# Kernel optimization log

Hardware: AMD Instinct MI355X
Metric: run time of the kernel (lower is better)

## Reference

```python
import math
import jax, jax.numpy as jnp
import numpy as np

B, S, D = 2, 2048, 512
H = 8
DPH = D // H
NEG = -1e18


def lorentz_linear(x, W, b, log_scale):
    """LorentzLinear with head_num=H: linear map then per-head projection onto the
    Lorentz hyperboloid: time = sigmoid(y0)*exp(scale)+1.1, space rescaled so that
    -time^2 + |space|^2 = -1 per head chunk."""
    Bx, Sx, Dx = x.shape
    y = (x @ W.T + b).reshape(Bx, Sx, H, DPH)
    time = jax.nn.sigmoid(y[..., :1]) * jnp.exp(log_scale) + 1.1
    space = y[..., 1:]
    sq = jnp.clip(jnp.sum(space * space, axis=-1, keepdims=True), 1e-8, None)
    scale = (time * time - 1.0) / sq
    out = jnp.concatenate([time, space * jnp.sqrt(scale)], axis=-1)
    return out.reshape(Bx, Sx, Dx)


def setup_inputs() -> dict:
    key0 = jax.random.key(0)
    ks = jax.random.split(key0, 8)
    std = 1.0 / np.sqrt(D)
    causal = ~jnp.tril(jnp.ones((S, S), dtype=bool))  # True = masked out
    return {
        "key": jax.random.normal(ks[0], (B, S, D), jnp.float32),
        "value": jax.random.normal(ks[1], (B, S, D), jnp.float32),
        "query": jax.random.normal(ks[2], (B, S, D), jnp.float32),
        "mask": jnp.broadcast_to(causal[None], (B, S, S)),
        "Wq": jax.random.normal(ks[3], (D, D), jnp.float32) * std,
        "bq": jnp.zeros((D,), jnp.float32),
        "sq": jnp.asarray(math.log(10.0), jnp.float32),
        "Wk": jax.random.normal(ks[4], (D, D), jnp.float32) * std,
        "bk": jnp.zeros((D,), jnp.float32),
        "sk": jnp.asarray(math.log(10.0), jnp.float32),
        "Wv": jax.random.normal(ks[5], (D, D), jnp.float32) * std,
        "bv": jnp.zeros((D,), jnp.float32),
        "sv": jnp.asarray(math.log(10.0), jnp.float32),
        "att_scale": jnp.full((1,), math.sqrt(D), jnp.float32),
        "att_bias": jnp.zeros((), jnp.float32),
    }


def reference(key, value, query, mask, Wq, bq, sq, Wk, bk, sk, Wv, bv, sv,
              att_scale, att_bias):
    def shape(x):  # (B,S,D) -> (B,H,S,dph)
        return x.reshape(B, -1, H, DPH).transpose(0, 2, 1, 3)

    q = shape(lorentz_linear(query, Wq, bq, sq))
    k = shape(lorentz_linear(key, Wk, bk, sk))
    v = shape(lorentz_linear(value, Wv, bv, sv))

    # Lorentz inner product <q,k>_L = -q0*k0 + q_space . k_space
    qm = jnp.concatenate([-q[..., :1], q[..., 1:]], axis=-1)
    cin = jnp.einsum('bhqd,bhkd->bhqk', qm, k)
    scores = (2.0 + 2.0 * cin) / att_scale + att_bias
    scores = jnp.where(mask[:, None], NEG, scores)
    attn = jax.nn.softmax(scores, axis=-1)  # (B,H,Q,K)

    # mid_point: weighted mean then renormalize to the hyperboloid
    ave = jnp.einsum('bhqk,bhkd->bhqd', attn, v)
    inner = -ave[..., :1] ** 2 + jnp.sum(ave[..., 1:] ** 2, axis=-1, keepdims=True)
    denom = jnp.sqrt(jnp.clip(jnp.abs(-inner), 1e-8, None))
    context = (ave / denom).transpose(0, 2, 1, 3)  # (B,Q,H,dph)
    return context, attn
```

## Files before the change

### kernel.cpp

```cpp
#include <hip/hip_runtime.h>
#include <math.h>

#define BB 2
#define SS 2048
#define DD 512
#define HH 8
#define MM (BB*SS)
#define CTX_ELEMS (MM*DD)

typedef __attribute__((ext_vector_type(8))) __bf16 bf16x8;
typedef __attribute__((ext_vector_type(4))) float  f32x4;

static __device__ inline unsigned short f2bf(float x) {
    unsigned u = __builtin_bit_cast(unsigned, x);
    u += 0x7fffu + ((u >> 16) & 1u);
    return (unsigned short)(u >> 16);
}
static __device__ inline float bf2f(unsigned short h) {
    unsigned u = ((unsigned)h) << 16;
    return __builtin_bit_cast(float, u);
}

static __device__ inline void unpack8(const uint4& a, const uint4& b, bf16x8& h, bf16x8& l) {
    uint4 hu, lu;
    hu.x = __builtin_amdgcn_perm(a.y, a.x, 0x05040100u);
    hu.y = __builtin_amdgcn_perm(a.w, a.z, 0x05040100u);
    hu.z = __builtin_amdgcn_perm(b.y, b.x, 0x05040100u);
    hu.w = __builtin_amdgcn_perm(b.w, b.z, 0x05040100u);
    lu.x = __builtin_amdgcn_perm(a.y, a.x, 0x07060302u);
    lu.y = __builtin_amdgcn_perm(a.w, a.z, 0x07060302u);
    lu.z = __builtin_amdgcn_perm(b.y, b.x, 0x07060302u);
    lu.w = __builtin_amdgcn_perm(b.w, b.z, 0x07060302u);
    h = __builtin_bit_cast(bf16x8, hu);
    l = __builtin_bit_cast(bf16x8, lu);
}

__global__ __launch_bounds__(256)
void lorentz_proj_mfma(const float* __restrict__ Xq, const float* __restrict__ Xk, const float* __restrict__ Xv,
                       const float* __restrict__ Wq, const float* __restrict__ bq, const float* __restrict__ sq,
                       const float* __restrict__ Wk, const float* __restrict__ bk, const float* __restrict__ sk,
                       const float* __restrict__ Wv, const float* __restrict__ bv, const float* __restrict__ sv,
                       float* __restrict__ oq, float* __restrict__ ok_, float* __restrict__ ov)
{
    __shared__ __align__(16) char sm[65536];
    char* Ah = sm;
    char* Al = sm + 16384;
    char* Bh = sm + 32768;
    char* Bl = sm + 49152;

    const float* X; const float* W; const float* bias; const float* ls; float* out;
    if (blockIdx.z == 0)      { X = Xq; W = Wq; bias = bq; ls = sq; out = oq;  }
    else if (blockIdx.z == 1) { X = Xk; W = Wk; bias = bk; ls = sk; out = ok_; }
    else                      { X = Xv; W = Wv; bias = bv; ls = sv; out = ov;  }

    const int tid = threadIdx.x;
    const int l63 = tid & 63;
    const int w   = tid >> 6;
    const int wm  = w >> 1;
    const int wn  = w & 1;
    const int lg  = l63 >> 4;
    const int ll  = l63 & 15;

    const int m0 = blockIdx.x << 7;
    const int n0 = blockIdx.y << 7;

    const int jr = tid >> 4;
    const int d0 = (tid & 15) << 2;

    f32x4 acc[4][4];
#pragma unroll
    for (int m = 0; m < 4; ++m)
#pragma unroll
        for (int n = 0; n < 4; ++n) acc[m][n] = (f32x4){0.f,0.f,0.f,0.f};

    for (int k0 = 0; k0 < DD; k0 += 64) {
        __syncthreads();
#pragma unroll
        for (int r = 0; r < 8; ++r) {
            const int row = jr + (r << 4);
            const int byte = ((row << 7) + (d0 << 1)) ^ ((row & 7) << 4);
            {
                const float4 x = *(const float4*)(X + (size_t)(m0 + row) * DD + k0 + d0);
                const unsigned short h0=f2bf(x.x), h1=f2bf(x.y), h2=f2bf(x.z), h3=f2bf(x.w);
                ushort4 hv = {h0,h1,h2,h3};
                ushort4 lv = {f2bf(x.x-bf2f(h0)), f2bf(x.y-bf2f(h1)), f2bf(x.z-bf2f(h2)), f2bf(x.w-bf2f(h3))};
                *(ushort4*)(Ah + byte) = hv;
                *(ushort4*)(Al + byte) = lv;
            }
            {
                const float4 x = *(const float4*)(W + (size_t)(n0 + row) * DD + k0 + d0);
                const unsigned short h0=f2bf(x.x), h1=f2bf(x.y), h2=f2bf(x.z), h3=f2bf(x.w);
                ushort4 hv = {h0,h1,h2,h3};
                ushort4 lv = {f2bf(x.x-bf2f(h0)), f2bf(x.y-bf2f(h1)), f2bf(x.z-bf2f(h2)), f2bf(x.w-bf2f(h3))};
                *(ushort4*)(Bh + byte) = hv;
                *(ushort4*)(Bl + byte) = lv;
            }
        }
        __syncthreads();

#pragma unroll
        for (int dc = 0; dc < 2; ++dc) {
            bf16x8 ah[4], al4[4], bh[4], bl4[4];
#pragma unroll
            for (int m = 0; m < 4; ++m) {
                const int q = (wm << 6) + (m << 4) + ll;
                const int byte = ((q << 7) + (dc << 6) + (lg << 4)) ^ ((q & 7) << 4);
                ah[m]  = *(const bf16x8*)(Ah + byte);
                al4[m] = *(const bf16x8*)(Al + byte);
            }
#pragma unroll
            for (int n = 0; n < 4; ++n) {
                const int q = (wn << 6) + (n << 4) + ll;
                const int byte = ((q << 7) + (dc << 6) + (lg << 4)) ^ ((q & 7) << 4);
                bh[n]  = *(const bf16x8*)(Bh + byte);
                bl4[n] = *(const bf16x8*)(Bl + byte);
            }
#pragma unroll
            for (int m = 0; m < 4; ++m)
#pragma unroll
                for (int n = 0; n < 4; ++n) {
                    acc[m][n] = __builtin_amdgcn_mfma_f32_16x16x32_bf16(ah[m],  bh[n],  acc[m][n], 0,0,0);
                    acc[m][n] = __builtin_amdgcn_mfma_f32_16x16x32_bf16(ah[m],  bl4[n], acc[m][n], 0,0,0);
                    acc[m][n] = __builtin_amdgcn_mfma_f32_16x16x32_bf16(al4[m], bh[n],  acc[m][n], 0,0,0);
                }
        }
    }

    const float es = expf(ls[0]);
    const int h = (blockIdx.y << 1) + wn;
    float bn[4];
#pragma unroll
    for (int n = 0; n < 4; ++n) bn[n] = bias[n0 + (wn << 6) + (n << 4) + ll];

#pragma unroll
    for (int m = 0; m < 4; ++m) {
#pragma unroll
        for (int reg = 0; reg < 4; ++reg) {
            float y[4];
            float part = 0.f;
#pragma unroll
            for (int n = 0; n < 4; ++n) {
                y[n] = acc[m][n][reg] + bn[n];
                const bool is_time = (n == 0) && (ll == 0);
                part += is_time ? 0.f : y[n]*y[n];
            }
            part += __shfl_xor(part, 1); part += __shfl_xor(part, 2);
            part += __shfl_xor(part, 4); part += __shfl_xor(part, 8);
            const float y0  = __shfl(y[0], (l63 & 48));
            const float tim = es / (1.f + expf(-y0)) + 1.1f;
            const float scf = sqrtf((tim*tim - 1.f) / fmaxf(part, 1e-8f));

            const int gr = m0 + (wm << 6) + (m << 4) + (lg << 2) + reg;
            const int b  = gr >> 11;
            const int s  = gr & (SS - 1);
            float* op = out + ((size_t)(b*HH + h)*SS + s) * 64;
#pragma unroll
            for (int n = 0; n < 4; ++n) {
                const int cih = (n << 4) + ll;
                op[cih] = (cih == 0) ? tim : y[n] * scf;
            }
        }
    }
}

__global__ __launch_bounds__(256)
void lorentz_attn_mfma(const float* __restrict__ qws, const float* __restrict__ kws, const float* __restrict__ vws,
                       const float* __restrict__ att_scale, const float* __restrict__ att_bias,
                       float* __restrict__ ctx, float* __restrict__ attn)
{
    __shared__ __align__(16) char sm[49152];
    char* Kh = sm;
    char* Kl = sm + 8192;
    char* Vp = sm + 16384;
    char* Pp = sm + 32768;
    char* Qh = Pp;
    char* Ql = Pp + 8192;

    const int tid = threadIdx.x;
    const int bh  = blockIdx.y;
    const int qt  = (bh >= 8) ? blockIdx.x : (31 - blockIdx.x);
    const int l63 = tid & 63;
    const int w   = tid >> 6;
    const int qoff = (w >> 1) << 5;
    const int joff = (w & 1) << 5;
    const int lg  = l63 >> 4;
    const int ll  = l63 & 15;

    const float inv_s = 1.f / att_scale[0];
    const float c1 = 2.f * inv_s;
    const float c0 = 2.f * inv_s + att_bias[0];

    const float* qb = qws + (size_t)bh * SS * 64;
    const float* kb = kws + (size_t)bh * SS * 64;
    const float* vb = vws + (size_t)bh * SS * 64;

    const int jr = tid >> 4;
    const int d0 = (tid & 15) << 2;

#pragma unroll
    for (int r = 0; r < 4; ++r) {
        const int j = jr + (r << 4);
        float4 x = *(const float4*)(qb + (size_t)(qt*64 + j)*64 + d0);
        if (d0 == 0) x.x = -x.x;
        const unsigned short h0=f2bf(x.x), h1=f2bf(x.y), h2=f2bf(x.z), h3=f2bf(x.w);
        ushort4 hv = {h0,h1,h2,h3};
        ushort4 lv = {f2bf(x.x-bf2f(h0)), f2bf(x.y-bf2f(h1)), f2bf(x.z-bf2f(h2)), f2bf(x.w-bf2f(h3))};
        const int byte = ((j<<7) + (d0<<1)) ^ ((j&7)<<4);
        *(ushort4*)(Qh + byte) = hv;
        *(ushort4*)(Ql + byte) = lv;
    }
    __syncthreads();

    bf16x8 qh[2][2], ql[2][2];
#pragma unroll
    for (int m = 0; m < 2; ++m)
#pragma unroll
        for (int dc = 0; dc < 2; ++dc) {
            const int q = qoff + (m<<4) + ll;
            const int byte = ((q<<7) + (dc<<6) + (lg<<4)) ^ ((q&7)<<4);
            qh[m][dc] = *(const bf16x8*)(Qh + byte);
            ql[m][dc] = *(const bf16x8*)(Ql + byte);
        }
    __syncthreads();

    float lrow[2][4] = {{0.f,0.f,0.f,0.f},{0.f,0.f,0.f,0.f}};

    for (int jt = 0; jt <= qt; ++jt) {
        __syncthreads();
#pragma unroll
        for (int r = 0; r < 4; ++r) {
            const int j = jr + (r << 4);
            const float4 x = *(const float4*)(kb + (size_t)(jt*64 + j)*64 + d0);
            const unsigned short h0=f2bf(x.x), h1=f2bf(x.y), h2=f2bf(x.z), h3=f2bf(x.w);
            ushort4 hv = {h0,h1,h2,h3};
            ushort4 lv = {f2bf(x.x-bf2f(h0)), f2bf(x.y-bf2f(h1)), f2bf(x.z-bf2f(h2)), f2bf(x.w-bf2f(h3))};
            const int byte = ((j<<7) + (d0<<1)) ^ ((j&7)<<4);
            *(ushort4*)(Kh + byte) = hv;
            *(ushort4*)(Kl + byte) = lv;
        }
        __syncthreads();

        f32x4 sacc[2][2];
#pragma unroll
        for (int m = 0; m < 2; ++m)
#pragma unroll
            for (int n = 0; n < 2; ++n) sacc[m][n] = (f32x4){0.f,0.f,0.f,0.f};
#pragma unroll
        for (int dc = 0; dc < 2; ++dc) {
            bf16x8 kh[2], kl[2];
#pragma unroll
            for (int n = 0; n < 2; ++n) {
                const int j = joff + (n<<4) + ll;
                const int byte = ((j<<7) + (dc<<6) + (lg<<4)) ^ ((j&7)<<4);
                kh[n] = *(const bf16x8*)(Kh + byte);
                kl[n] = *(const bf16x8*)(Kl + byte);
            }
#pragma unroll
            for (int m = 0; m < 2; ++m)
#pragma unroll
                for (int n = 0; n < 2; ++n) {
                    sacc[m][n] = __builtin_amdgcn_mfma_f32_16x16x32_bf16(qh[m][dc], kh[n], sacc[m][n], 0,0,0);
                    sacc[m][n] = __builtin_amdgcn_mfma_f32_16x16x32_bf16(qh[m][dc], kl[n], sacc[m][n], 0,0,0);
                    sacc[m][n] = __builtin_amdgcn_mfma_f32_16x16x32_bf16(ql[m][dc], kh[n], sacc[m][n], 0,0,0);
                }
        }

        const bool diag = (jt == qt);
#pragma unroll
        for (int m = 0; m < 2; ++m)
#pragma unroll
            for (int reg = 0; reg < 4; ++reg) {
                const int ri = qoff + (m<<4) + (lg<<2) + reg;
                float rs = 0.f;
#pragma unroll
                for (int n = 0; n < 2; ++n) {
                    const int cj = joff + (n<<4) + ll;
                    const float sc = sacc[m][n][reg] * c1 + c0;
                    rs += (!diag || cj <= ri) ? __expf(sc) : 0.f;
                }
                rs += __shfl_xor(rs, 1); rs += __shfl_xor(rs, 2);
                rs += __shfl_xor(rs, 4); rs += __shfl_xor(rs, 8);
                lrow[m][reg] += rs;
            }
    }

    __syncthreads();
    {
        float* dred = (float*)sm;
        if (ll == 0) {
#pragma unroll
            for (int m = 0; m < 2; ++m)
#pragma unroll
                for (int reg = 0; reg < 4; ++reg)
                    dred[(qoff + (m<<4) + (lg<<2) + reg)*2 + (w & 1)] = lrow[m][reg];
        }
        __syncthreads();
#pragma unroll
        for (int m = 0; m < 2; ++m)
#pragma unroll
            for (int reg = 0; reg < 4; ++reg) {
                const int ri = qoff + (m<<4) + (lg<<2) + reg;
                lrow[m][reg] = dred[ri*2] + dred[ri*2 + 1];
            }
    }

    float il[2][4];
#pragma unroll
    for (int m = 0; m < 2; ++m)
#pragma unroll
        for (int reg = 0; reg < 4; ++reg) il[m][reg] = 1.f / lrow[m][reg];

    f32x4 oacc[2][2];
#pragma unroll
    for (int m = 0; m < 2; ++m)
#pragma unroll
        for (int n = 0; n < 2; ++n) oacc[m][n] = (f32x4){0.f,0.f,0.f,0.f};

    for (int jt = 0; jt <= qt; ++jt) {
        __syncthreads();
#pragma unroll
        for (int r = 0; r < 4; ++r) {
            const int j = jr + (r << 4);
            const float4 x = *(const float4*)(kb + (size_t)(jt*64 + j)*64 + d0);
            const unsigned short h0=f2bf(x.x), h1=f2bf(x.y), h2=f2bf(x.z), h3=f2bf(x.w);
            ushort4 hv = {h0,h1,h2,h3};
            ushort4 lv = {f2bf(x.x-bf2f(h0)), f2bf(x.y-bf2f(h1)), f2bf(x.z-bf2f(h2)), f2bf(x.w-bf2f(h3))};
            const int byte = ((j<<7) + (d0<<1)) ^ ((j&7)<<4);
            *(ushort4*)(Kh + byte) = hv;
            *(ushort4*)(Kl + byte) = lv;

            const float4 v = *(const float4*)(vb + (size_t)(jt*64 + j)*64 + d0);
            const float vs[4] = {v.x, v.y, v.z, v.w};
#pragma unroll
            for (int c = 0; c < 4; ++c) {
                const int d = d0 + c;
                const unsigned short vh = f2bf(vs[c]);
                const unsigned short vlo = f2bf(vs[c] - bf2f(vh));
                const int vbyte = ((d<<8) + (j<<2)) ^ ((d&7)<<4);
                *(unsigned*)(Vp + vbyte) = (unsigned)vh | ((unsigned)vlo << 16);
            }
        }
        __syncthreads();

        f32x4 sacc[2][2];
#pragma unroll
        for (int m = 0; m < 2; ++m)
#pragma unroll
            for (int n = 0; n < 2; ++n) sacc[m][n] = (f32x4){0.f,0.f,0.f,0.f};
#pragma unroll
        for (int dc = 0; dc < 2; ++dc) {
            bf16x8 kh[2], kl[2];
#pragma unroll
            for (int n = 0; n < 2; ++n) {
                const int j = joff + (n<<4) + ll;
                const int byte = ((j<<7) + (dc<<6) + (lg<<4)) ^ ((j&7)<<4);
                kh[n] = *(const bf16x8*)(Kh + byte);
                kl[n] = *(const bf16x8*)(Kl + byte);
            }
#pragma unroll
            for (int m = 0; m < 2; ++m)
#pragma unroll
                for (int n = 0; n < 2; ++n) {
                    sacc[m][n] = __builtin_amdgcn_mfma_f32_16x16x32_bf16(qh[m][dc], kh[n], sacc[m][n], 0,0,0);
                    sacc[m][n] = __builtin_amdgcn_mfma_f32_16x16x32_bf16(qh[m][dc], kl[n], sacc[m][n], 0,0,0);
                    sacc[m][n] = __builtin_amdgcn_mfma_f32_16x16x32_bf16(ql[m][dc], kh[n], sacc[m][n], 0,0,0);
                }
        }

        const bool diag = (jt == qt);
#pragma unroll
        for (int m = 0; m < 2; ++m)
#pragma unroll
            for (int reg = 0; reg < 4; ++reg) {
                const int ri = qoff + (m<<4) + (lg<<2) + reg;
                const int gi = (qt<<6) + ri;
#pragma unroll
                for (int n = 0; n < 2; ++n) {
                    const int cj = joff + (n<<4) + ll;
                    const float sc = sacc[m][n][reg] * c1 + c0;
                    const float p = (!diag || cj <= ri) ? __expf(sc) : 0.f;
                    const float pn = p * il[m][reg];
                    attn[((size_t)bh*SS + gi)*SS + (jt<<6) + cj] = pn;
                    const unsigned short ph = f2bf(pn);
                    const unsigned short pl = f2bf(pn - bf2f(ph));
                    const int byte = ((ri<<8) + (cj<<2)) ^ ((ri&7)<<4);
                    *(unsigned*)(Pp + byte) = (unsigned)ph | ((unsigned)pl << 16);
                }
            }
        __syncthreads();

#pragma unroll
        for (int jc = 0; jc < 2; ++jc) {
            bf16x8 pah[2], pal[2], vfh[2], vfl[2];
            const int jbase4 = ((jc<<5) + (lg<<3)) << 2;
#pragma unroll
            for (int m = 0; m < 2; ++m) {
                const int q = qoff + (m<<4) + ll;
                const int X = (q<<8) + jbase4;
                const int s = (q&7)<<4;
                const uint4 a = *(const uint4*)(Pp + (X ^ s));
                const uint4 b = *(const uint4*)(Pp + ((X + 16) ^ s));
                unpack8(a, b, pah[m], pal[m]);
            }
#pragma unroll
            for (int n = 0; n < 2; ++n) {
                const int d = joff + (n<<4) + ll;
                const int X = (d<<8) + jbase4;
                const int s = (d&7)<<4;
                const uint4 a = *(const uint4*)(Vp + (X ^ s));
                const uint4 b = *(const uint4*)(Vp + ((X + 16) ^ s));
                unpack8(a, b, vfh[n], vfl[n]);
            }
#pragma unroll
            for (int m = 0; m < 2; ++m)
#pragma unroll
                for (int n = 0; n < 2; ++n) {
                    oacc[m][n] = __builtin_amdgcn_mfma_f32_16x16x32_bf16(pah[m], vfh[n], oacc[m][n], 0,0,0);
                    oacc[m][n] = __builtin_amdgcn_mfma_f32_16x16x32_bf16(pah[m], vfl[n], oacc[m][n], 0,0,0);
                    oacc[m][n] = __builtin_amdgcn_mfma_f32_16x16x32_bf16(pal[m], vfh[n], oacc[m][n], 0,0,0);
                }
        }
    }

    {
        const int cstart = (qt + 1) << 6;
        const float4 z = make_float4(0.f, 0.f, 0.f, 0.f);
        for (int r = 0; r < 64; ++r) {
            float* rowp = attn + ((size_t)bh*SS + (qt<<6) + r)*SS;
            for (int c = cstart + (tid << 2); c < SS; c += 1024)
                *(float4*)(rowp + c) = z;
        }
    }

    float part[2][4];
#pragma unroll
    for (int m = 0; m < 2; ++m)
#pragma unroll
        for (int reg = 0; reg < 4; ++reg) {
            float s = 0.f;
#pragma unroll
            for (int n = 0; n < 2; ++n) {
                const int d = joff + (n<<4) + ll;
                const float av = oacc[m][n][reg] * il[m][reg];
                s += (d == 0) ? -av*av : av*av;
            }
            s += __shfl_xor(s, 1); s += __shfl_xor(s, 2);
            s += __shfl_xor(s, 4); s += __shfl_xor(s, 8);
            part[m][reg] = s;
        }
    __syncthreads();
    float* red = (float*)sm;
    if (ll == 0) {
#pragma unroll
        for (int m = 0; m < 2; ++m)
#pragma unroll
            for (int reg = 0; reg < 4; ++reg)
                red[(qoff + (m<<4) + (lg<<2) + reg)*2 + (w & 1)] = part[m][reg];
    }
    __syncthreads();

    const int b = bh >> 3, h = bh & 7;
#pragma unroll
    for (int m = 0; m < 2; ++m)
#pragma unroll
        for (int reg = 0; reg < 4; ++reg) {
            const int ri = qoff + (m<<4) + (lg<<2) + reg;
            const float inner = red[ri*2] + red[ri*2 + 1];
            const float dinv = 1.f / sqrtf(fmaxf(fabsf(inner), 1e-8f));
            const int gi = (qt<<6) + ri;
#pragma unroll
            for (int n = 0; n < 2; ++n) {
                const int d = joff + (n<<4) + ll;
                const float av = oacc[m][n][reg] * il[m][reg];
                ctx[((size_t)(b*SS + gi)*HH + h)*64 + d] = av * dinv;
            }
        }
}

extern "C" void kernel_launch(void* const* d_in, const int* in_sizes, int n_in,
                              void* d_out, int out_size, void* d_ws, size_t ws_size,
                              hipStream_t stream)
{
    const float* key   = (const float*)d_in[0];
    const float* value = (const float*)d_in[1];
    const float* query = (const float*)d_in[2];
    const float* Wq = (const float*)d_in[4];
    const float* bq = (const float*)d_in[5];
    const float* sq = (const float*)d_in[6];
    const float* Wk = (const float*)d_in[7];
    const float* bk = (const float*)d_in[8];
    const float* sk = (const float*)d_in[9];
    const float* Wv = (const float*)d_in[10];
    const float* bv = (const float*)d_in[11];
    const float* sv = (const float*)d_in[12];
    const float* as_ = (const float*)d_in[13];
    const float* ab  = (const float*)d_in[14];

    float* ws  = (float*)d_ws;
    float* qws = ws;
    float* kws = ws + (size_t)CTX_ELEMS;
    float* vws = ws + (size_t)2 * CTX_ELEMS;

    float* ctx  = (float*)d_out;
    float* attn = ctx + (size_t)CTX_ELEMS;

    dim3 pgrid(MM / 128, DD / 128, 3);
    lorentz_proj_mfma<<<pgrid, 256, 0, stream>>>(query, key, value,
                                                 Wq, bq, sq, Wk, bk, sk, Wv, bv, sv,
                                                 qws, kws, vws);

    dim3 agrid(32, BB * HH);
    lorentz_attn_mfma<<<agrid, 256, 0, stream>>>(qws, kws, vws, as_, ab, ctx, attn);
}
```

Before: 558.4 us.

## Split attention tile across eight waves instead of four

Doubles the attention block from 256 to 512 threads, with each wave now owning a 32x16 sub-tile of the 64x64 score and output tiles instead of 32x32. K/V staging loops, row-sum reductions (now across four column waves) and the attn zero-fill stride are adjusted to match. The aim is more waves per block to hide latency, since the grid is only 512 blocks, at the cost of more barrier participants and extra shared-memory reduction traffic.

```diff
diff --git a/kernel.cpp b/kernel.cpp
--- a/kernel.cpp
+++ b/kernel.cpp
@@ -163,7 +163,7 @@
     }
 }
 
-__global__ __launch_bounds__(256)
+__global__ __launch_bounds__(512, 4)
 void lorentz_attn_mfma(const float* __restrict__ qws, const float* __restrict__ kws, const float* __restrict__ vws,
                        const float* __restrict__ att_scale, const float* __restrict__ att_bias,
                        float* __restrict__ ctx, float* __restrict__ attn)
@@ -179,12 +179,14 @@
     const int tid = threadIdx.x;
     const int bh  = blockIdx.y;
     const int qt  = (bh >= 8) ? blockIdx.x : (31 - blockIdx.x);
-    const int l63 = tid & 63;
-    const int w   = tid >> 6;
-    const int qoff = (w >> 1) << 5;
-    const int joff = (w & 1) << 5;
-    const int lg  = l63 >> 4;
-    const int ll  = l63 & 15;
+    const int lane = tid & 63;
+    const int w    = tid >> 6;
+    const int wq   = w >> 2;
+    const int wj   = w & 3;
+    const int qoff = wq << 5;
+    const int joff = wj << 4;
+    const int lg   = lane >> 4;
+    const int ll   = lane & 15;
 
     const float inv_s = 1.f / att_scale[0];
     const float c1 = 2.f * inv_s;
@@ -198,8 +200,8 @@
     const int d0 = (tid & 15) << 2;
 
 #pragma unroll
-    for (int r = 0; r < 4; ++r) {
-        const int j = jr + (r << 4);
+    for (int r = 0; r < 2; ++r) {
+        const int j = jr + (r << 5);
         float4 x = *(const float4*)(qb + (size_t)(qt*64 + j)*64 + d0);
         if (d0 == 0) x.x = -x.x;
         const unsigned short h0=f2bf(x.x), h1=f2bf(x.y), h2=f2bf(x.z), h3=f2bf(x.w);
@@ -228,8 +230,8 @@
     for (int jt = 0; jt <= qt; ++jt) {
         __syncthreads();
 #pragma unroll
-        for (int r = 0; r < 4; ++r) {
-            const int j = jr + (r << 4);
+        for (int r = 0; r < 2; ++r) {
+            const int j = jr + (r << 5);
             const float4 x = *(const float4*)(kb + (size_t)(jt*64 + j)*64 + d0);
             const unsigned short h0=f2bf(x.x), h1=f2bf(x.y), h2=f2bf(x.z), h3=f2bf(x.w);
             ushort4 hv = {h0,h1,h2,h3};
@@ -240,29 +242,21 @@
         }
         __syncthreads();
 
-        f32x4 sacc[2][2];
-#pragma unroll
-        for (int m = 0; m < 2; ++m)
-#pragma unroll
-            for (int n = 0; n < 2; ++n) sacc[m][n] = (f32x4){0.f,0.f,0.f,0.f};
+        f32x4 sacc[2];
+#pragma unroll
+        for (int m = 0; m < 2; ++m) sacc[m] = (f32x4){0.f,0.f,0.f,0.f};
 #pragma unroll
         for (int dc = 0; dc < 2; ++dc) {
-            bf16x8 kh[2], kl[2];
-#pragma unroll
-            for (int n = 0; n < 2; ++n) {
-                const int j = joff + (n<<4) + ll;
-                const int byte = ((j<<7) + (dc<<6) + (lg<<4)) ^ ((j&7)<<4);
-                kh[n] = *(const bf16x8*)(Kh + byte);
-                kl[n] = *(const bf16x8*)(Kl + byte);
-            }
-#pragma unroll
-            for (int m = 0; m < 2; ++m)
-#pragma unroll
-                for (int n = 0; n < 2; ++n) {
-                    sacc[m][n] = __builtin_amdgcn_mfma_f32_16x16x32_bf16(qh[m][dc], kh[n], sacc[m][n], 0,0,0);
-                    sacc[m][n] = __builtin_amdgcn_mfma_f32_16x16x32_bf16(qh[m][dc], kl[n], sacc[m][n], 0,0,0);
-                    sacc[m][n] = __builtin_amdgcn_mfma_f32_16x16x32_bf16(ql[m][dc], kh[n], sacc[m][n], 0,0,0);
-                }
+            const int j = joff + ll;
+            const int byte = ((j<<7) + (dc<<6) + (lg<<4)) ^ ((j&7)<<4);
+            const bf16x8 kh = *(const bf16x8*)(Kh + byte);
+            const bf16x8 kl = *(const bf16x8*)(Kl + byte);
+#pragma unroll
+            for (int m = 0; m < 2; ++m) {
+                sacc[m] = __builtin_amdgcn_mfma_f32_16x16x32_bf16(qh[m][dc], kh, sacc[m], 0,0,0);
+                sacc[m] = __builtin_amdgcn_mfma_f32_16x16x32_bf16(qh[m][dc], kl, sacc[m], 0,0,0);
+                sacc[m] = __builtin_amdgcn_mfma_f32_16x16x32_bf16(ql[m][dc], kh, sacc[m], 0,0,0);
+            }
         }
 
         const bool diag = (jt == qt);
@@ -271,13 +265,9 @@
 #pragma unroll
             for (int reg = 0; reg < 4; ++reg) {
                 const int ri = qoff + (m<<4) + (lg<<2) + reg;
-                float rs = 0.f;
-#pragma unroll
-                for (int n = 0; n < 2; ++n) {
-                    const int cj = joff + (n<<4) + ll;
-                    const float sc = sacc[m][n][reg] * c1 + c0;
-                    rs += (!diag || cj <= ri) ? __expf(sc) : 0.f;
-                }
+                const int cj = joff + ll;
+                const float sc = sacc[m][reg] * c1 + c0;
+                float rs = (!diag || cj <= ri) ? __expf(sc) : 0.f;
                 rs += __shfl_xor(rs, 1); rs += __shfl_xor(rs, 2);
                 rs += __shfl_xor(rs, 4); rs += __shfl_xor(rs, 8);
                 lrow[m][reg] += rs;
@@ -292,7 +282,7 @@
             for (int m = 0; m < 2; ++m)
 #pragma unroll
                 for (int reg = 0; reg < 4; ++reg)
-                    dred[(qoff + (m<<4) + (lg<<2) + reg)*2 + (w & 1)] = lrow[m][reg];
+                    dred[((qoff + (m<<4) + (lg<<2) + reg)<<2) + wj] = lrow[m][reg];
         }
         __syncthreads();
 #pragma unroll
@@ -300,7 +290,7 @@
 #pragma unroll
             for (int reg = 0; reg < 4; ++reg) {
                 const int ri = qoff + (m<<4) + (lg<<2) + reg;
-                lrow[m][reg] = dred[ri*2] + dred[ri*2 + 1];
+                lrow[m][reg] = dred[(ri<<2)] + dred[(ri<<2)+1] + dred[(ri<<2)+2] + dred[(ri<<2)+3];
             }
     }
 
@@ -310,17 +300,15 @@
 #pragma unroll
         for (int reg = 0; reg < 4; ++reg) il[m][reg] = 1.f / lrow[m][reg];
 
-    f32x4 oacc[2][2];
-#pragma unroll
-    for (int m = 0; m < 2; ++m)
-#pragma unroll
-        for (int n = 0; n < 2; ++n) oacc[m][n] = (f32x4){0.f,0.f,0.f,0.f};
+    f32x4 oacc[2];
+#pragma unroll
+    for (int m = 0; m < 2; ++m) oacc[m] = (f32x4){0.f,0.f,0.f,0.f};
 
     for (int jt = 0; jt <= qt; ++jt) {
         __syncthreads();
 #pragma unroll
-        for (int r = 0; r < 4; ++r) {
-            const int j = jr + (r << 4);
+        for (int r = 0; r < 2; ++r) {
+            const int j = jr + (r << 5);
             const float4 x = *(const float4*)(kb + (size_t)(jt*64 + j)*64 + d0);
             const unsigned short h0=f2bf(x.x), h1=f2bf(x.y), h2=f2bf(x.z), h3=f2bf(x.w);
             ushort4 hv = {h0,h1,h2,h3};
@@ -342,29 +330,21 @@
         }
         __syncthreads();
 
-        f32x4 sacc[2][2];
-#pragma unroll
-        for (int m = 0; m < 2; ++m)
-#pragma unroll
-            for (int n = 0; n < 2; ++n) sacc[m][n] = (f32x4){0.f,0.f,0.f,0.f};
+        f32x4 sacc[2];
+#pragma unroll
+        for (int m = 0; m < 2; ++m) sacc[m] = (f32x4){0.f,0.f,0.f,0.f};
 #pragma unroll
         for (int dc = 0; dc < 2; ++dc) {
-            bf16x8 kh[2], kl[2];
-#pragma unroll
-            for (int n = 0; n < 2; ++n) {
-                const int j = joff + (n<<4) + ll;
-                const int byte = ((j<<7) + (dc<<6) + (lg<<4)) ^ ((j&7)<<4);
-                kh[n] = *(const bf16x8*)(Kh + byte);
-                kl[n] = *(const bf16x8*)(Kl + byte);
-            }
-#pragma unroll
-            for (int m = 0; m < 2; ++m)
-#pragma unroll
-                for (int n = 0; n < 2; ++n) {
-                    sacc[m][n] = __builtin_amdgcn_mfma_f32_16x16x32_bf16(qh[m][dc], kh[n], sacc[m][n], 0,0,0);
-                    sacc[m][n] = __builtin_amdgcn_mfma_f32_16x16x32_bf16(qh[m][dc], kl[n], sacc[m][n], 0,0,0);
-                    sacc[m][n] = __builtin_amdgcn_mfma_f32_16x16x32_bf16(ql[m][dc], kh[n], sacc[m][n], 0,0,0);
-                }
+            const int j = joff + ll;
+            const int byte = ((j<<7) + (dc<<6) + (lg<<4)) ^ ((j&7)<<4);
+            const bf16x8 kh = *(const bf16x8*)(Kh + byte);
+            const bf16x8 kl = *(const bf16x8*)(Kl + byte);
+#pragma unroll
+            for (int m = 0; m < 2; ++m) {
+                sacc[m] = __builtin_amdgcn_mfma_f32_16x16x32_bf16(qh[m][dc], kh, sacc[m], 0,0,0);
+                sacc[m] = __builtin_amdgcn_mfma_f32_16x16x32_bf16(qh[m][dc], kl, sacc[m], 0,0,0);
+                sacc[m] = __builtin_amdgcn_mfma_f32_16x16x32_bf16(ql[m][dc], kh, sacc[m], 0,0,0);
+            }
         }
 
         const bool diag = (jt == qt);
@@ -374,24 +354,21 @@
             for (int reg = 0; reg < 4; ++reg) {
                 const int ri = qoff + (m<<4) + (lg<<2) + reg;
                 const int gi = (qt<<6) + ri;
-#pragma unroll
-                for (int n = 0; n < 2; ++n) {
-                    const int cj = joff + (n<<4) + ll;
-                    const float sc = sacc[m][n][reg] * c1 + c0;
-                    const float p = (!diag || cj <= ri) ? __expf(sc) : 0.f;
-                    const float pn = p * il[m][reg];
-                    attn[((size_t)bh*SS + gi)*SS + (jt<<6) + cj] = pn;
-                    const unsigned short ph = f2bf(pn);
-                    const unsigned short pl = f2bf(pn - bf2f(ph));
-                    const int byte = ((ri<<8) + (cj<<2)) ^ ((ri&7)<<4);
-                    *(unsigned*)(Pp + byte) = (unsigned)ph | ((unsigned)pl << 16);
-                }
+                const int cj = joff + ll;
+                const float sc = sacc[m][reg] * c1 + c0;
+                const float p = (!diag || cj <= ri) ? __expf(sc) : 0.f;
+                const float pn = p * il[m][reg];
+                attn[((size_t)bh*SS + gi)*SS + (jt<<6) + cj] = pn;
+                const unsigned short ph = f2bf(pn);
+                const unsigned short pl = f2bf(pn - bf2f(ph));
+                const int byte = ((ri<<8) + (cj<<2)) ^ ((ri&7)<<4);
+                *(unsigned*)(Pp + byte) = (unsigned)ph | ((unsigned)pl << 16);
             }
         __syncthreads();
 
 #pragma unroll
         for (int jc = 0; jc < 2; ++jc) {
-            bf16x8 pah[2], pal[2], vfh[2], vfl[2];
+            bf16x8 pah[2], pal[2], vfh, vfl;
             const int jbase4 = ((jc<<5) + (lg<<3)) << 2;
 #pragma unroll
             for (int m = 0; m < 2; ++m) {
@@ -402,23 +379,20 @@
                 const uint4 b = *(const uint4*)(Pp + ((X + 16) ^ s));
                 unpack8(a, b, pah[m], pal[m]);
             }
-#pragma unroll
-            for (int n = 0; n < 2; ++n) {
-                const int d = joff + (n<<4) + ll;
+            {
+                const int d = joff + ll;
                 const int X = (d<<8) + jbase4;
                 const int s = (d&7)<<4;
                 const uint4 a = *(const uint4*)(Vp + (X ^ s));
                 const uint4 b = *(const uint4*)(Vp + ((X + 16) ^ s));
-                unpack8(a, b, vfh[n], vfl[n]);
-            }
-#pragma unroll
-            for (int m = 0; m < 2; ++m)
-#pragma unroll
-                for (int n = 0; n < 2; ++n) {
-                    oacc[m][n] = __builtin_amdgcn_mfma_f32_16x16x32_bf16(pah[m], vfh[n], oacc[m][n], 0,0,0);
-                    oacc[m][n] = __builtin_amdgcn_mfma_f32_16x16x32_bf16(pah[m], vfl[n], oacc[m][n], 0,0,0);
-                    oacc[m][n] = __builtin_amdgcn_mfma_f32_16x16x32_bf16(pal[m], vfh[n], oacc[m][n], 0,0,0);
-                }
+                unpack8(a, b, vfh, vfl);
+            }
+#pragma unroll
+            for (int m = 0; m < 2; ++m) {
+                oacc[m] = __builtin_amdgcn_mfma_f32_16x16x32_bf16(pah[m], vfh, oacc[m], 0,0,0);
+                oacc[m] = __builtin_amdgcn_mfma_f32_16x16x32_bf16(pah[m], vfl, oacc[m], 0,0,0);
+                oacc[m] = __builtin_amdgcn_mfma_f32_16x16x32_bf16(pal[m], vfh, oacc[m], 0,0,0);
+            }
         }
     }
 
@@ -427,7 +401,7 @@
         const float4 z = make_float4(0.f, 0.f, 0.f, 0.f);
         for (int r = 0; r < 64; ++r) {
             float* rowp = attn + ((size_t)bh*SS + (qt<<6) + r)*SS;
-            for (int c = cstart + (tid << 2); c < SS; c += 1024)
+            for (int c = cstart + (tid << 2); c < SS; c += 2048)
                 *(float4*)(rowp + c) = z;
         }
     }
@@ -437,13 +411,9 @@
     for (int m = 0; m < 2; ++m)
 #pragma unroll
         for (int reg = 0; reg < 4; ++reg) {
-            float s = 0.f;
-#pragma unroll
-            for (int n = 0; n < 2; ++n) {
-                const int d = joff + (n<<4) + ll;
-                const float av = oacc[m][n][reg] * il[m][reg];
-                s += (d == 0) ? -av*av : av*av;
-            }
+            const int d = joff + ll;
+            const float av = oacc[m][reg] * il[m][reg];
+            float s = (d == 0) ? -av*av : av*av;
             s += __shfl_xor(s, 1); s += __shfl_xor(s, 2);
             s += __shfl_xor(s, 4); s += __shfl_xor(s, 8);
             part[m][reg] = s;
@@ -455,7 +425,7 @@
         for (int m = 0; m < 2; ++m)
 #pragma unroll
             for (int reg = 0; reg < 4; ++reg)
-                red[(qoff + (m<<4) + (lg<<2) + reg)*2 + (w & 1)] = part[m][reg];
+                red[((qoff + (m<<4) + (lg<<2) + reg)<<2) + wj] = part[m][reg];
     }
     __syncthreads();
 
@@ -465,15 +435,12 @@
 #pragma unroll
         for (int reg = 0; reg < 4; ++reg) {
             const int ri = qoff + (m<<4) + (lg<<2) + reg;
-            const float inner = red[ri*2] + red[ri*2 + 1];
+            const float inner = red[(ri<<2)] + red[(ri<<2)+1] + red[(ri<<2)+2] + red[(ri<<2)+3];
             const float dinv = 1.f / sqrtf(fmaxf(fabsf(inner), 1e-8f));
             const int gi = (qt<<6) + ri;
-#pragma unroll
-            for (int n = 0; n < 2; ++n) {
-                const int d = joff + (n<<4) + ll;
-                const float av = oacc[m][n][reg] * il[m][reg];
-                ctx[((size_t)(b*SS + gi)*HH + h)*64 + d] = av * dinv;
-            }
+            const int d = joff + ll;
+            const float av = oacc[m][reg] * il[m][reg];
+            ctx[((size_t)(b*SS + gi)*HH + h)*64 + d] = av * dinv;
         }
 }
 
@@ -510,5 +477,5 @@
                                                  qws, kws, vws);
 
     dim3 agrid(32, BB * HH);
-    lorentz_attn_mfma<<<agrid, 256, 0, stream>>>(qws, kws, vws, as_, ab, ctx, attn);
-}
+    lorentz_attn_mfma<<<agrid, 512, 0, stream>>>(qws, kws, vws, as_, ab, ctx, attn);
+}
```

After: 555.2 us. About the same (-0.6%).
